# Kernel tuning notes

Measured on AMD Instinct MI355X. Metric: run time of the kernel, lower is better.

Reference implementation:

```python
import jax, jax.numpy as jnp
import numpy as np


def setup_inputs() -> dict:
    key = jax.random.key(0)
    k1, k2, k3 = jax.random.split(key, 3)
    B, C, H, W = 8, 256, 64, 64
    K = jax.random.normal(k1, (B, C, H, W), dtype=jnp.float32)
    Q = jax.random.normal(k2, (B, C, H, W), dtype=jnp.float32)
    V = jax.random.normal(k3, (B, C, H, W), dtype=jnp.float32)
    return {"K": K, "Q": Q, "V": V}


def reference(K, Q, V):
    # K, Q: [b, dim, h, w]; V: [b, v_dim, h, w]
    b, dim, h, w = K.shape
    v_dim = V.shape[1]
    hw = h * w
    Qf = jnp.transpose(K.reshape(b, dim, hw), (0, 2, 1)) * 0  # placeholder removed below
    Qf = jnp.transpose(Q.reshape(b, dim, hw), (0, 2, 1))  # [b, hw, dim]
    Kf = K.reshape(b, dim, hw)                              # [b, dim, hw]
    Vf = jnp.transpose(V.reshape(b, v_dim, hw), (0, 2, 1))  # [b, hw, v_dim]
    scores = jnp.einsum('bqd,bdk->bqk', Qf, Kf)             # [b, hw_q, hw_k]
    # NOTE: softmax over the QUERY axis (dim=1), matching the torch code
    att = jax.nn.softmax(scores, axis=1)
    out = jnp.einsum('bqk,bkv->bqv', att, Vf)               # [b, hw, v_dim]
    out = out.reshape(b, h, w, v_dim)
    return jnp.transpose(out, (0, 3, 1, 2))                 # [b, v_dim, h, w]
```

## Files before the change

### kernel.cpp

```cpp
#include <hip/hip_runtime.h>

#define HW   4096
#define DIM  256
#define NB   8

typedef short bf16x8 __attribute__((ext_vector_type(8)));
typedef short s16x4  __attribute__((ext_vector_type(4)));
typedef float f32x4  __attribute__((ext_vector_type(4)));
typedef float f32x16 __attribute__((ext_vector_type(16)));
typedef unsigned int u32_g __attribute__((address_space(1)));
typedef unsigned int u32_l __attribute__((address_space(3)));

__device__ __forceinline__ void split_bf16(float x, short& hi, short& lo) {
    unsigned u  = __builtin_bit_cast(unsigned, x);
    unsigned rh = (u + 0x7FFFu + ((u >> 16) & 1u)) >> 16;
    hi = (short)rh;
    float hf  = __builtin_bit_cast(float, rh << 16);
    float rem = x - hf;
    unsigned u2 = __builtin_bit_cast(unsigned, rem);
    unsigned rl = (u2 + 0x7FFFu + ((u2 >> 16) & 1u)) >> 16;
    lo = (short)rl;
}

__device__ __forceinline__ f32x4 mfma16(bf16x8 a, bf16x8 b, f32x4 c) {
    return __builtin_amdgcn_mfma_f32_16x16x32_bf16(a, b, c, 0, 0, 0);
}
__device__ __forceinline__ f32x16 mfma32(bf16x8 a, bf16x8 b, f32x16 c) {
    return __builtin_amdgcn_mfma_f32_32x32x16_bf16(a, b, c, 0, 0, 0);
}

__device__ __forceinline__ void gload16(const void* g, void* l) {
    __builtin_amdgcn_global_load_lds((const u32_g*)g, (u32_l*)l, 16, 0, 0);
}
__device__ __forceinline__ void gload4(const void* g, void* l) {
    __builtin_amdgcn_global_load_lds((const u32_g*)g, (u32_l*)l, 4, 0, 0);
}

extern "C" __global__ void __launch_bounds__(256)
pass0_T(const float* __restrict__ src, short* __restrict__ dsth,
        short* __restrict__ dstl)
{
    __shared__ __attribute__((aligned(16))) short TH[16][264];
    __shared__ __attribute__((aligned(16))) short TL[16][264];
    const int b   = blockIdx.y;
    const int hw0 = blockIdx.x * 16;
    const int t   = threadIdx.x;
    const float* sb = src + (size_t)b * DIM * HW;

    {
        const int rl = t & 15;
        const int dl = t >> 4;
        #pragma unroll
        for (int dp = 0; dp < 16; ++dp) {
            int d = dl + dp * 16;
            float x = sb[(size_t)d * HW + hw0 + rl];
            short h, l; split_bf16(x, h, l);
            TH[rl][d] = h; TL[rl][d] = l;
        }
    }
    __syncthreads();

    const int r   = t >> 4;
    const int c0  = (t & 15) * 2;
    const int swz = (r & 7) << 4;
    size_t rowbyte = ((size_t)b * HW + hw0 + r) * (size_t)(DIM * 2);
    char* dh = (char*)dsth + rowbyte;
    char* dl = (char*)dstl + rowbyte;
    #pragma unroll
    for (int j = 0; j < 2; ++j) {
        int cb  = (c0 + j) * 16;
        int cbs = cb ^ swz;
        *(f32x4*)(dh + cbs) = *(const f32x4*)((const char*)&TH[r][0] + cb);
        *(f32x4*)(dl + cbs) = *(const f32x4*)((const char*)&TL[r][0] + cb);
    }
}

extern "C" __global__ void __launch_bounds__(256)
pass0_V(const float* __restrict__ V, short* __restrict__ v2)
{
    const int b = blockIdx.y, v = blockIdx.x, t = threadIdx.x;
    const float* sv = V + ((size_t)b * DIM + v) * HW + t * 16;
    #pragma unroll
    for (int s = 0; s < 2; ++s) {
        f32x4 x0 = *(const f32x4*)(sv + s * 8);
        f32x4 x1 = *(const f32x4*)(sv + s * 8 + 4);
        s16x4 h0, l0, h1, l1;
        #pragma unroll
        for (int j = 0; j < 4; ++j) {
            short h, l;
            split_bf16(x0[j], h, l); h0[j] = h; l0[j] = l;
            split_bf16(x1[j], h, l); h1[j] = h; l1[j] = l;
        }
        short* dp = v2 + (((size_t)b * 512 + (size_t)(t * 2 + s)) * DIM + v) * 16;
        *(s16x4*)(dp + 0)  = h0;
        *(s16x4*)(dp + 4)  = h1;
        *(s16x4*)(dp + 8)  = l0;
        *(s16x4*)(dp + 12) = l1;
    }
}

extern "C" __global__ void __launch_bounds__(512, 2)
k4_stats(const short* __restrict__ KTh, const short* __restrict__ KTl,
         const short* __restrict__ QTh, const short* __restrict__ QTl,
         float* __restrict__ m_out, float* __restrict__ il_out)
{
    __shared__ __attribute__((aligned(16))) short QH[2][64][256];
    __shared__ __attribute__((aligned(16))) short QL[2][64][256];
    __shared__ __attribute__((aligned(16))) float MRG[2][128][2];

    const int id   = blockIdx.x;
    const int b    = id & 7;
    const int k0b  = (id >> 3) * 128;
    const int t    = threadIdx.x;
    const int lane = t & 63;
    const int w    = t >> 6;
    const int l32  = lane & 31;
    const int g2   = lane >> 5;
    const int wk   = w >> 1;
    const int wq   = w & 1;

    bf16x8 kh[16], kl[16];
    {
        const int krow = k0b + wk * 32 + l32;
        const char* rh = (const char*)KTh + ((size_t)b * HW + krow) * 512;
        const char* rl = (const char*)KTl + ((size_t)b * HW + krow) * 512;
        const int swz = (l32 & 7) << 4;
        #pragma unroll
        for (int s = 0; s < 16; ++s) {
            int cb = (s * 32 + g2 * 16) ^ swz;
            kh[s] = *(const bf16x8*)(rh + cb);
            kl[s] = *(const bf16x8*)(rl + cb);
        }
    }

    const char* qhbase = (const char*)QTh + (size_t)b * HW * 512;
    const char* qlbase = (const char*)QTl + (size_t)b * HW * 512;
    auto stage = [&](int bi, int q0) {
        #pragma unroll
        for (int j = 0; j < 4; ++j) {
            int cc = (j << 3) + w;
            int o  = cc * 1024;
            gload16(qhbase + (size_t)q0 * 512 + o + lane * 16,
                    (char*)&QH[bi][0][0] + o);
            gload16(qlbase + (size_t)q0 * 512 + o + lane * 16,
                    (char*)&QL[bi][0][0] + o);
        }
    };

    float mr[16], lr[16];
    #pragma unroll
    for (int r = 0; r < 16; ++r) { mr[r] = -3.0e38f; lr[r] = 0.0f; }

    stage(0, 0);
    __syncthreads();

    const int qrow = wq * 32 + l32;
    const int qswz = (qrow & 7) << 4;

    for (int it = 0; it < 64; ++it) {
        const int cur = it & 1;
        if (it + 1 < 64) stage(cur ^ 1, (it + 1) * 64);

        const char* bhr = (const char*)&QH[cur][qrow][0];
        const char* blr = (const char*)&QL[cur][qrow][0];
        f32x16 c1, c2;
        #pragma unroll
        for (int e = 0; e < 16; ++e) { c1[e] = 0.0f; c2[e] = 0.0f; }

        __builtin_amdgcn_s_setprio(1);
        #pragma unroll
        for (int s = 0; s < 16; ++s) {
            int cb = (s * 32 + g2 * 16) ^ qswz;
            bf16x8 bh = *(const bf16x8*)(bhr + cb);
            bf16x8 bl = *(const bf16x8*)(blr + cb);
            c1 = mfma32(kh[s], bh, c1);
            c1 = mfma32(kh[s], bl, c1);
            c2 = mfma32(kl[s], bh, c2);
        }
        __builtin_amdgcn_s_setprio(0);

        #pragma unroll
        for (int r = 0; r < 16; ++r) {
            float sv = c1[r] + c2[r];
            float nm = fmaxf(mr[r], sv);
            lr[r] = lr[r] * __expf(mr[r] - nm) + __expf(sv - nm);
            mr[r] = nm;
        }
        __syncthreads();
    }

    #pragma unroll
    for (int r = 0; r < 16; ++r) {
        float m = mr[r], l = lr[r];
        #pragma unroll
        for (int off = 1; off < 32; off <<= 1) {
            float m2 = __shfl_xor(m, off);
            float l2 = __shfl_xor(l, off);
            float nm = fmaxf(m, m2);
            l = l * __expf(m - nm) + l2 * __expf(m2 - nm);
            m = nm;
        }
        mr[r] = m; lr[r] = l;
    }
    if (l32 == 0) {
        #pragma unroll
        for (int r = 0; r < 16; ++r) {
            int klo = wk * 32 + 4 * g2 + (r & 3) + 8 * (r >> 2);
            MRG[wq][klo][0] = mr[r];
            MRG[wq][klo][1] = lr[r];
        }
    }
    __syncthreads();
    if (t < 128) {
        float m0 = MRG[0][t][0], l0 = MRG[0][t][1];
        float m1 = MRG[1][t][0], l1 = MRG[1][t][1];
        float nm = fmaxf(m0, m1);
        float l  = l0 * __expf(m0 - nm) + l1 * __expf(m1 - nm);
        m_out[b * HW + k0b + t]  = nm;
        il_out[b * HW + k0b + t] = 1.0f / l;
    }
}

extern "C" __global__ void __launch_bounds__(512, 2)
k4_out(const short* __restrict__ KTh, const short* __restrict__ KTl,
       const short* __restrict__ QTh, const short* __restrict__ QTl,
       const short* __restrict__ V2,
       const float* __restrict__ m_in, const float* __restrict__ il_in,
       float* __restrict__ out)
{
    __shared__ __attribute__((aligned(16))) short KH[64][256];
    __shared__ __attribute__((aligned(16))) short KL[64][256];
    __shared__ __attribute__((aligned(16))) short PH[128][72];
    __shared__ __attribute__((aligned(16))) short PL[128][72];
    __shared__ __attribute__((aligned(16))) float MI[2][128];

    const int id   = blockIdx.x;
    const int b    = id & 7;
    const int q0   = (id >> 3) * 128;
    const int t    = threadIdx.x;
    const int lane = t & 63;
    const int w    = t >> 6;
    const int l32  = lane & 31;
    const int g2   = lane >> 5;
    const int a    = w & 1;
    const int c    = w >> 1;
    const int wv   = w >> 1;
    const int wq2  = w & 1;

    bf16x8 qh[16], ql[16];
    {
        const int qrow = q0 + c * 32 + l32;
        const char* rh = (const char*)QTh + ((size_t)b * HW + qrow) * 512;
        const char* rl = (const char*)QTl + ((size_t)b * HW + qrow) * 512;
        const int swz = (l32 & 7) << 4;
        #pragma unroll
        for (int s = 0; s < 16; ++s) {
            int cb = (s * 32 + g2 * 16) ^ swz;
            qh[s] = *(const bf16x8*)(rh + cb);
            ql[s] = *(const bf16x8*)(rl + cb);
        }
    }

    const char* khbase = (const char*)KTh + (size_t)b * HW * 512;
    const char* klbase = (const char*)KTl + (size_t)b * HW * 512;
    auto stageK = [&](int k0s) {
        #pragma unroll
        for (int j = 0; j < 4; ++j) {
            int cc = (j << 3) + w;
            int o  = cc * 1024;
            gload16(khbase + (size_t)k0s * 512 + o + lane * 16,
                    (char*)&KH[0][0] + o);
            gload16(klbase + (size_t)k0s * 512 + o + lane * 16,
                    (char*)&KL[0][0] + o);
        }
    };
    const float* mB  = m_in  + b * HW;
    const float* ilB = il_in + b * HW;
    auto stageMI = [&](int bi, int k0s) {
        if (w == 0) {
            gload4(mB  + k0s + lane, (char*)&MI[bi][0]);
            gload4(ilB + k0s + lane, (char*)&MI[bi][64]);
        }
    };

    f32x16 acc[2][2];
    #pragma unroll
    for (int i = 0; i < 2; ++i)
        #pragma unroll
        for (int j = 0; j < 2; ++j)
            #pragma unroll
            for (int e = 0; e < 16; ++e) acc[i][j][e] = 0.0f;

    stageK(0);
    stageMI(0, 0);
    __syncthreads();

    const int arow = a * 32 + l32;
    const int aswz = (l32 & 7) << 4;
    const char* ahr = (const char*)&KH[arow][0];
    const char* alr = (const char*)&KL[arow][0];
    const int prow = c * 32 + l32;

    for (int it = 0; it < 64; ++it) {
        const int cur = it & 1;
        const int k0  = it * 64;

        f32x16 c1, c2;
        #pragma unroll
        for (int e = 0; e < 16; ++e) { c1[e] = 0.0f; c2[e] = 0.0f; }

        __builtin_amdgcn_s_setprio(1);
        #pragma unroll
        for (int s = 0; s < 16; ++s) {
            int cb = (s * 32 + g2 * 16) ^ aswz;
            bf16x8 ah = *(const bf16x8*)(ahr + cb);
            bf16x8 al = *(const bf16x8*)(alr + cb);
            c1 = mfma32(ah, qh[s], c1);
            c1 = mfma32(ah, ql[s], c1);
            c2 = mfma32(al, qh[s], c2);
        }
        __builtin_amdgcn_s_setprio(0);

        __syncthreads();

        if (it + 1 < 64) {
            stageK(k0 + 64);
            stageMI(cur ^ 1, k0 + 64);
        }

        #pragma unroll
        for (int run = 0; run < 4; ++run) {
            int idx = a * 32 + 4 * g2 + 8 * run;
            f32x4 m4 = *(const f32x4*)&MI[cur][idx];
            f32x4 i4 = *(const f32x4*)&MI[cur][64 + idx];
            s16x4 ph, pl;
            #pragma unroll
            for (int e = 0; e < 4; ++e) {
                int r = run * 4 + e;
                float sv = c1[r] + c2[r];
                float p  = __expf(sv - m4[e]) * i4[e];
                short h, l; split_bf16(p, h, l);
                ph[e] = h; pl[e] = l;
            }
            *(s16x4*)&PH[prow][idx] = ph;
            *(s16x4*)&PL[prow][idx] = pl;
        }

        __syncthreads();

        __builtin_amdgcn_s_setprio(1);
        #pragma unroll
        for (int kc = 0; kc < 4; ++kc) {
            bf16x8 pbh[2], pbl[2];
            #pragma unroll
            for (int qt = 0; qt < 2; ++qt) {
                int pr = wq2 * 64 + qt * 32 + l32;
                pbh[qt] = *(const bf16x8*)&PH[pr][kc * 16 + g2 * 8];
                pbl[qt] = *(const bf16x8*)&PL[pr][kc * 16 + g2 * 8];
            }
            const int seg = it * 8 + kc * 2 + g2;
            #pragma unroll
            for (int mt = 0; mt < 2; ++mt) {
                int v = wv * 64 + mt * 32 + l32;
                const short* vp = V2 + (((size_t)b * 512 + seg) * DIM + v) * 16;
                bf16x8 vh = *(const bf16x8*)(vp);
                bf16x8 vl = *(const bf16x8*)(vp + 8);
                #pragma unroll
                for (int qt = 0; qt < 2; ++qt) {
                    acc[mt][qt] = mfma32(vh, pbh[qt], acc[mt][qt]);
                    acc[mt][qt] = mfma32(vh, pbl[qt], acc[mt][qt]);
                    acc[mt][qt] = mfma32(vl, pbh[qt], acc[mt][qt]);
                }
            }
        }
        __builtin_amdgcn_s_setprio(0);
    }

    float* __restrict__ ob = out + (size_t)b * DIM * HW;
    #pragma unroll
    for (int mt = 0; mt < 2; ++mt)
        #pragma unroll
        for (int qt = 0; qt < 2; ++qt)
            #pragma unroll
            for (int r = 0; r < 16; ++r) {
                int v = wv * 64 + mt * 32 + (r & 3) + 8 * (r >> 2) + 4 * g2;
                int q = q0 + wq2 * 64 + qt * 32 + l32;
                ob[(size_t)v * HW + q] = acc[mt][qt][r];
            }
}

extern "C" __global__ void __launch_bounds__(256, 1)
k_stats(const float* __restrict__ K, const float* __restrict__ Q,
        float* __restrict__ m_out, float* __restrict__ il_out)
{
    __shared__ __attribute__((aligned(16))) short KtH[64][264];
    __shared__ __attribute__((aligned(16))) short KtL[64][264];
    __shared__ __attribute__((aligned(16))) short QtH[32][264];
    __shared__ __attribute__((aligned(16))) short QtL[32][264];

    const int b = blockIdx.y, k0 = blockIdx.x * 64, t = threadIdx.x;
    const int lane = t & 63, w = t >> 6, g = lane >> 4, lq = lane & 15;
    const float* Kb = K + (size_t)b * DIM * HW;
    const float* Qb = Q + (size_t)b * DIM * HW;

    {
        const int kk = t & 63, d0 = t >> 6;
        #pragma unroll 4
        for (int pass = 0; pass < 64; ++pass) {
            int d = d0 + pass * 4;
            float x = Kb[(size_t)d * HW + k0 + kk];
            short h, l; split_bf16(x, h, l);
            KtH[kk][d] = h; KtL[kk][d] = l;
        }
    }
    float mr[4], lr[4];
    #pragma unroll
    for (int r = 0; r < 4; ++r) { mr[r] = -3.0e38f; lr[r] = 0.0f; }

    for (int q0 = 0; q0 < HW; q0 += 32) {
        __syncthreads();
        {
            const int qq = t & 31, d0 = t >> 5;
            #pragma unroll 4
            for (int pass = 0; pass < 32; ++pass) {
                int d = d0 + pass * 8;
                float x = Qb[(size_t)d * HW + q0 + qq];
                short h, l; split_bf16(x, h, l);
                QtH[qq][d] = h; QtL[qq][d] = l;
            }
        }
        __syncthreads();
        #pragma unroll
        for (int qt = 0; qt < 2; ++qt) {
            f32x4 acc = {0.f, 0.f, 0.f, 0.f};
            #pragma unroll
            for (int ds = 0; ds < 8; ++ds) {
                const int dof = ds * 32 + g * 8;
                bf16x8 ah = *(const bf16x8*)&KtH[w * 16 + lq][dof];
                bf16x8 al = *(const bf16x8*)&KtL[w * 16 + lq][dof];
                bf16x8 bh = *(const bf16x8*)&QtH[qt * 16 + lq][dof];
                bf16x8 bl = *(const bf16x8*)&QtL[qt * 16 + lq][dof];
                acc = mfma16(ah, bh, acc);
                acc = mfma16(ah, bl, acc);
                acc = mfma16(al, bh, acc);
            }
            #pragma unroll
            for (int r = 0; r < 4; ++r) {
                float s = acc[r];
                if (s > mr[r]) { lr[r] = lr[r] * __expf(mr[r] - s) + 1.0f; mr[r] = s; }
                else lr[r] += __expf(s - mr[r]);
            }
        }
    }
    #pragma unroll
    for (int r = 0; r < 4; ++r) {
        float m = mr[r], l = lr[r];
        #pragma unroll
        for (int off = 1; off < 16; off <<= 1) {
            float m2 = __shfl_xor(m, off), l2 = __shfl_xor(l, off);
            float mn = fmaxf(m, m2);
            l = l * __expf(m - mn) + l2 * __expf(m2 - mn);
            m = mn;
        }
        if (lq == 0) {
            int kg = k0 + w * 16 + g * 4 + r;
            m_out[b * HW + kg] = m;
            il_out[b * HW + kg] = 1.0f / l;
        }
    }
}

extern "C" __global__ void __launch_bounds__(256, 1)
k_attn_out(const float* __restrict__ K, const float* __restrict__ Q,
           const float* __restrict__ V,
           const float* __restrict__ m_in, const float* __restrict__ il_in,
           float* __restrict__ out)
{
    __shared__ __attribute__((aligned(16))) short QtH[64][264];
    __shared__ __attribute__((aligned(16))) short QtL[64][264];
    __shared__ __attribute__((aligned(16))) short KtH[32][264];
    __shared__ __attribute__((aligned(16))) short KtL[32][264];
    __shared__ __attribute__((aligned(16))) short PtH[64][40];
    __shared__ __attribute__((aligned(16))) short PtL[64][40];

    const int b = blockIdx.y, q0 = blockIdx.x * 64, t = threadIdx.x;
    const int lane = t & 63, w = t >> 6, g = lane >> 4, lq = lane & 15;
    const int g2 = lane >> 5, l32 = lane & 31;
    const float* Kb = K + (size_t)b * DIM * HW;
    const float* Qb = Q + (size_t)b * DIM * HW;
    const float* Vb = V + (size_t)b * DIM * HW;
    const float* mB = m_in + b * HW;
    const float* ilB = il_in + b * HW;

    {
        const int qq = t & 63, d0 = t >> 6;
        #pragma unroll 4
        for (int pass = 0; pass < 64; ++pass) {
            int d = d0 + pass * 4;
            float x = Qb[(size_t)d * HW + q0 + qq];
            short h, l; split_bf16(x, h, l);
            QtH[qq][d] = h; QtL[qq][d] = l;
        }
    }
    f32x16 acc[2][2];
    #pragma unroll
    for (int i = 0; i < 2; ++i)
        #pragma unroll
        for (int j = 0; j < 2; ++j)
            #pragma unroll
            for (int e = 0; e < 16; ++e) acc[i][j][e] = 0.0f;

    for (int k0 = 0; k0 < HW; k0 += 32) {
        __syncthreads();
        {
            const int kk = t & 31, d0 = t >> 5;
            #pragma unroll 4
            for (int pass = 0; pass < 32; ++pass) {
                int d = d0 + pass * 8;
                float x = Kb[(size_t)d * HW + k0 + kk];
                short h, l; split_bf16(x, h, l);
                KtH[kk][d] = h; KtL[kk][d] = l;
            }
        }
        __syncthreads();
        f32x4 sacc[2];
        #pragma unroll
        for (int kt = 0; kt < 2; ++kt) { f32x4 z = {0.f,0.f,0.f,0.f}; sacc[kt] = z; }
        #pragma unroll
        for (int ds = 0; ds < 8; ++ds) {
            const int dof = ds * 32 + g * 8;
            bf16x8 bh = *(const bf16x8*)&QtH[w * 16 + lq][dof];
            bf16x8 bl = *(const bf16x8*)&QtL[w * 16 + lq][dof];
            #pragma unroll
            for (int kt = 0; kt < 2; ++kt) {
                bf16x8 ah = *(const bf16x8*)&KtH[kt * 16 + lq][dof];
                bf16x8 al = *(const bf16x8*)&KtL[kt * 16 + lq][dof];
                sacc[kt] = mfma16(ah, bh, sacc[kt]);
                sacc[kt] = mfma16(ah, bl, sacc[kt]);
                sacc[kt] = mfma16(al, bh, sacc[kt]);
            }
        }
        {
            const int qc = w * 16 + lq;
            #pragma unroll
            for (int kt = 0; kt < 2; ++kt) {
                s16x4 ph, pl;
                #pragma unroll
                for (int r = 0; r < 4; ++r) {
                    int kg = k0 + kt * 16 + g * 4 + r;
                    float p = __expf(sacc[kt][r] - mB[kg]) * ilB[kg];
                    short h, l; split_bf16(p, h, l);
                    ph[r] = h; pl[r] = l;
                }
                *(s16x4*)&PtH[qc][kt * 16 + g * 4] = ph;
                *(s16x4*)&PtL[qc][kt * 16 + g * 4] = pl;
            }
        }
        __syncthreads();
        #pragma unroll
        for (int kc = 0; kc < 2; ++kc) {
            bf16x8 pbh[2], pbl[2];
            #pragma unroll
            for (int qt = 0; qt < 2; ++qt) {
                pbh[qt] = *(const bf16x8*)&PtH[qt * 32 + l32][kc * 16 + g2 * 8];
                pbl[qt] = *(const bf16x8*)&PtL[qt * 32 + l32][kc * 16 + g2 * 8];
            }
            #pragma unroll
            for (int mt = 0; mt < 2; ++mt) {
                const int v = w * 64 + mt * 32 + l32;
                const float* vp = Vb + (size_t)v * HW + k0 + kc * 16 + g2 * 8;
                f32x4 x0 = *(const f32x4*)vp;
                f32x4 x1 = *(const f32x4*)(vp + 4);
                bf16x8 ah, al;
                #pragma unroll
                for (int j = 0; j < 4; ++j) {
                    short h, l;
                    split_bf16(x0[j], h, l); ah[j] = h;     al[j] = l;
                    split_bf16(x1[j], h, l); ah[4 + j] = h; al[4 + j] = l;
                }
                #pragma unroll
                for (int qt = 0; qt < 2; ++qt) {
                    acc[mt][qt] = mfma32(ah, pbh[qt], acc[mt][qt]);
                    acc[mt][qt] = mfma32(ah, pbl[qt], acc[mt][qt]);
                    acc[mt][qt] = mfma32(al, pbh[qt], acc[mt][qt]);
                }
            }
        }
    }
    float* ob = out + (size_t)b * DIM * HW;
    #pragma unroll
    for (int mt = 0; mt < 2; ++mt)
        #pragma unroll
        for (int qt = 0; qt < 2; ++qt)
            #pragma unroll
            for (int r = 0; r < 16; ++r) {
                int v = w * 64 + mt * 32 + (r & 3) + 8 * (r >> 2) + 4 * g2;
                int q = q0 + qt * 32 + l32;
                ob[(size_t)v * HW + q] = acc[mt][qt][r];
            }
}

extern "C" void kernel_launch(void* const* d_in, const int* in_sizes, int n_in,
                              void* d_out, int out_size, void* d_ws, size_t ws_size,
                              hipStream_t stream)
{
    (void)in_sizes; (void)n_in; (void)out_size;
    const float* K = (const float*)d_in[0];
    const float* Q = (const float*)d_in[1];
    const float* V = (const float*)d_in[2];

    char* wsb = (char*)d_ws;
    float* m_ws  = (float*)wsb;
    float* il_ws = m_ws + (size_t)NB * HW;

    const size_t planeElems = (size_t)NB * HW * DIM;
    const size_t statsBytes = 262144;
    const size_t need = statsBytes + planeElems * 2 * 4
                                   + planeElems * 2 * 2 ;

    dim3 blk(256);
    if (ws_size >= need) {
        short* KTh = (short*)(wsb + statsBytes);
        short* KTl = KTh + planeElems;
        short* QTh = KTl + planeElems;
        short* QTl = QTh + planeElems;
        short* V2  = QTl + planeElems;

        dim3 gT(HW / 16, NB);
        pass0_T<<<gT, blk, 0, stream>>>(K, KTh, KTl);
        pass0_T<<<gT, blk, 0, stream>>>(Q, QTh, QTl);
        dim3 gV(DIM, NB);
        pass0_V<<<gV, blk, 0, stream>>>(V, V2);

        dim3 blk5(512);
        k4_stats<<<dim3(256), blk5, 0, stream>>>(KTh, KTl, QTh, QTl, m_ws, il_ws);
        k4_out<<<dim3(256), blk5, 0, stream>>>(KTh, KTl, QTh, QTl, V2,
                                               m_ws, il_ws, (float*)d_out);
    } else {
        dim3 gM(64, NB);
        k_stats<<<gM, blk, 0, stream>>>(K, Q, m_ws, il_ws);
        k_attn_out<<<gM, blk, 0, stream>>>(K, Q, V, m_ws, il_ws, (float*)d_out);
    }
}
```

Baseline: 710.3 us.

## Stream low-bf16 planes from global in registers, double-buffer K tile in out kernel

The stats and output kernels stop staging the low bf16 half of Q/K in LDS. Instead each wave reads it straight from global memory into registers in groups of four, interleaved with the MFMA chain. This halves LDS traffic and footprint, and the freed space lets the output kernel double-buffer the high K tile so the next tile's prefetch is issued before the current QK compute instead of after a barrier. Other changes: the two score accumulators merge into one, and the P tile row pitch is padded to 68 with split 8-byte LDS reads. The risk is global-load latency stalling the MFMA chain and extra L2 traffic, since each wave re-reads the same low rows.

```diff
diff --git a/kernel.cpp b/kernel.cpp
--- a/kernel.cpp
+++ b/kernel.cpp
@@ -100,12 +100,11 @@
 }
 
 extern "C" __global__ void __launch_bounds__(512, 2)
-k4_stats(const short* __restrict__ KTh, const short* __restrict__ KTl,
+k6_stats(const short* __restrict__ KTh, const short* __restrict__ KTl,
          const short* __restrict__ QTh, const short* __restrict__ QTl,
          float* __restrict__ m_out, float* __restrict__ il_out)
 {
     __shared__ __attribute__((aligned(16))) short QH[2][64][256];
-    __shared__ __attribute__((aligned(16))) short QL[2][64][256];
     __shared__ __attribute__((aligned(16))) float MRG[2][128][2];
 
     const int id   = blockIdx.x;
@@ -135,15 +134,25 @@
 
     const char* qhbase = (const char*)QTh + (size_t)b * HW * 512;
     const char* qlbase = (const char*)QTl + (size_t)b * HW * 512;
-    auto stage = [&](int bi, int q0) {
+    auto stage = [&](int bi, int q0s) {
         #pragma unroll
         for (int j = 0; j < 4; ++j) {
             int cc = (j << 3) + w;
             int o  = cc * 1024;
-            gload16(qhbase + (size_t)q0 * 512 + o + lane * 16,
+            gload16(qhbase + (size_t)q0s * 512 + o + lane * 16,
                     (char*)&QH[bi][0][0] + o);
-            gload16(qlbase + (size_t)q0 * 512 + o + lane * 16,
-                    (char*)&QL[bi][0][0] + o);
+        }
+    };
+
+    const int qrow = wq * 32 + l32;
+    const int qswz = (qrow & 7) << 4;
+
+    auto LOADB = [&](bf16x8* buf, int sg, const char* rowp) {
+        #pragma unroll
+        for (int e = 0; e < 4; ++e) {
+            const int s = sg * 4 + e;
+            int cb = (s * 32 + g2 * 16) ^ qswz;
+            buf[e] = *(const bf16x8*)(rowp + cb);
         }
     };
 
@@ -153,35 +162,44 @@
 
     stage(0, 0);
     __syncthreads();
-
-    const int qrow = wq * 32 + l32;
-    const int qswz = (qrow & 7) << 4;
 
     for (int it = 0; it < 64; ++it) {
         const int cur = it & 1;
         if (it + 1 < 64) stage(cur ^ 1, (it + 1) * 64);
 
-        const char* bhr = (const char*)&QH[cur][qrow][0];
-        const char* blr = (const char*)&QL[cur][qrow][0];
-        f32x16 c1, c2;
-        #pragma unroll
-        for (int e = 0; e < 16; ++e) { c1[e] = 0.0f; c2[e] = 0.0f; }
+        const char* blrow = qlbase + (size_t)(it * 64 + qrow) * 512;
+        const char* bhr   = (const char*)&QH[cur][qrow][0];
+
+        bf16x8 blA[4], blB[4];
+        LOADB(blA, 0, blrow);
+        LOADB(blB, 1, blrow);
+
+        f32x16 cS;
+        #pragma unroll
+        for (int e = 0; e < 16; ++e) cS[e] = 0.0f;
+
+        auto SGRP = [&](const bf16x8* blbuf, int sg) {
+            #pragma unroll
+            for (int e = 0; e < 4; ++e) {
+                const int s = sg * 4 + e;
+                int cb = (s * 32 + g2 * 16) ^ qswz;
+                bf16x8 bh = *(const bf16x8*)(bhr + cb);
+                cS = mfma32(kh[s], bh, cS);
+                cS = mfma32(kh[s], blbuf[e], cS);
+                cS = mfma32(kl[s], bh, cS);
+            }
+        };
 
         __builtin_amdgcn_s_setprio(1);
-        #pragma unroll
-        for (int s = 0; s < 16; ++s) {
-            int cb = (s * 32 + g2 * 16) ^ qswz;
-            bf16x8 bh = *(const bf16x8*)(bhr + cb);
-            bf16x8 bl = *(const bf16x8*)(blr + cb);
-            c1 = mfma32(kh[s], bh, c1);
-            c1 = mfma32(kh[s], bl, c1);
-            c2 = mfma32(kl[s], bh, c2);
-        }
+        SGRP(blA, 0); LOADB(blA, 2, blrow);
+        SGRP(blB, 1); LOADB(blB, 3, blrow);
+        SGRP(blA, 2);
+        SGRP(blB, 3);
         __builtin_amdgcn_s_setprio(0);
 
         #pragma unroll
         for (int r = 0; r < 16; ++r) {
-            float sv = c1[r] + c2[r];
+            float sv = cS[r];
             float nm = fmaxf(mr[r], sv);
             lr[r] = lr[r] * __expf(mr[r] - nm) + __expf(sv - nm);
             mr[r] = nm;
@@ -222,16 +240,15 @@
 }
 
 extern "C" __global__ void __launch_bounds__(512, 2)
-k4_out(const short* __restrict__ KTh, const short* __restrict__ KTl,
+k6_out(const short* __restrict__ KTh, const short* __restrict__ KTl,
        const short* __restrict__ QTh, const short* __restrict__ QTl,
        const short* __restrict__ V2,
        const float* __restrict__ m_in, const float* __restrict__ il_in,
        float* __restrict__ out)
 {
-    __shared__ __attribute__((aligned(16))) short KH[64][256];
-    __shared__ __attribute__((aligned(16))) short KL[64][256];
-    __shared__ __attribute__((aligned(16))) short PH[128][72];
-    __shared__ __attribute__((aligned(16))) short PL[128][72];
+    __shared__ __attribute__((aligned(16))) short KH[2][64][256];
+    __shared__ __attribute__((aligned(16))) short PH[128][68];
+    __shared__ __attribute__((aligned(16))) short PL[128][68];
     __shared__ __attribute__((aligned(16))) float MI[2][128];
 
     const int id   = blockIdx.x;
@@ -263,15 +280,13 @@
 
     const char* khbase = (const char*)KTh + (size_t)b * HW * 512;
     const char* klbase = (const char*)KTl + (size_t)b * HW * 512;
-    auto stageK = [&](int k0s) {
+    auto stageK = [&](int bi, int k0s) {
         #pragma unroll
         for (int j = 0; j < 4; ++j) {
             int cc = (j << 3) + w;
             int o  = cc * 1024;
             gload16(khbase + (size_t)k0s * 512 + o + lane * 16,
-                    (char*)&KH[0][0] + o);
-            gload16(klbase + (size_t)k0s * 512 + o + lane * 16,
-                    (char*)&KL[0][0] + o);
+                    (char*)&KH[bi][0][0] + o);
         }
     };
     const float* mB  = m_in  + b * HW;
@@ -291,42 +306,62 @@
             #pragma unroll
             for (int e = 0; e < 16; ++e) acc[i][j][e] = 0.0f;
 
-    stageK(0);
+    stageK(0, 0);
     stageMI(0, 0);
     __syncthreads();
 
     const int arow = a * 32 + l32;
     const int aswz = (l32 & 7) << 4;
-    const char* ahr = (const char*)&KH[arow][0];
-    const char* alr = (const char*)&KL[arow][0];
     const int prow = c * 32 + l32;
+
+    auto LOADA = [&](bf16x8* buf, int sg, const char* rowp) {
+        #pragma unroll
+        for (int e = 0; e < 4; ++e) {
+            const int s = sg * 4 + e;
+            int cb = (s * 32 + g2 * 16) ^ aswz;
+            buf[e] = *(const bf16x8*)(rowp + cb);
+        }
+    };
 
     for (int it = 0; it < 64; ++it) {
         const int cur = it & 1;
         const int k0  = it * 64;
 
-        f32x16 c1, c2;
-        #pragma unroll
-        for (int e = 0; e < 16; ++e) { c1[e] = 0.0f; c2[e] = 0.0f; }
+        if (it + 1 < 64) {
+            stageK(cur ^ 1, k0 + 64);
+            stageMI(cur ^ 1, k0 + 64);
+        }
+
+        const char* alrow = klbase + (size_t)(k0 + arow) * 512;
+        bf16x8 alA[4], alB[4];
+        LOADA(alA, 0, alrow);
+        LOADA(alB, 1, alrow);
+
+        const char* ahr = (const char*)&KH[cur][arow][0];
+        f32x16 cS;
+        #pragma unroll
+        for (int e = 0; e < 16; ++e) cS[e] = 0.0f;
+
+        auto SGRP = [&](const bf16x8* albuf, int sg) {
+            #pragma unroll
+            for (int e = 0; e < 4; ++e) {
+                const int s = sg * 4 + e;
+                int cb = (s * 32 + g2 * 16) ^ aswz;
+                bf16x8 ah = *(const bf16x8*)(ahr + cb);
+                cS = mfma32(ah, qh[s], cS);
+                cS = mfma32(ah, ql[s], cS);
+                cS = mfma32(albuf[e], qh[s], cS);
+            }
+        };
 
         __builtin_amdgcn_s_setprio(1);
-        #pragma unroll
-        for (int s = 0; s < 16; ++s) {
-            int cb = (s * 32 + g2 * 16) ^ aswz;
-            bf16x8 ah = *(const bf16x8*)(ahr + cb);
-            bf16x8 al = *(const bf16x8*)(alr + cb);
-            c1 = mfma32(ah, qh[s], c1);
-            c1 = mfma32(ah, ql[s], c1);
-            c2 = mfma32(al, qh[s], c2);
-        }
+        SGRP(alA, 0); LOADA(alA, 2, alrow);
+        SGRP(alB, 1); LOADA(alB, 3, alrow);
+        SGRP(alA, 2);
+        SGRP(alB, 3);
         __builtin_amdgcn_s_setprio(0);
 
         __syncthreads();
-
-        if (it + 1 < 64) {
-            stageK(k0 + 64);
-            stageMI(cur ^ 1, k0 + 64);
-        }
 
         #pragma unroll
         for (int run = 0; run < 4; ++run) {
@@ -337,8 +372,7 @@
             #pragma unroll
             for (int e = 0; e < 4; ++e) {
                 int r = run * 4 + e;
-                float sv = c1[r] + c2[r];
-                float p  = __expf(sv - m4[e]) * i4[e];
+                float p = __expf(cS[r] - m4[e]) * i4[e];
                 short h, l; split_bf16(p, h, l);
                 ph[e] = h; pl[e] = l;
             }
@@ -355,8 +389,14 @@
             #pragma unroll
             for (int qt = 0; qt < 2; ++qt) {
                 int pr = wq2 * 64 + qt * 32 + l32;
-                pbh[qt] = *(const bf16x8*)&PH[pr][kc * 16 + g2 * 8];
-                pbl[qt] = *(const bf16x8*)&PL[pr][kc * 16 + g2 * 8];
+                const short* p0 = &PH[pr][kc * 16 + g2 * 8];
+                const short* p1 = &PL[pr][kc * 16 + g2 * 8];
+                s16x4 a0 = *(const s16x4*)(p0);
+                s16x4 a1 = *(const s16x4*)(p0 + 4);
+                s16x4 b0 = *(const s16x4*)(p1);
+                s16x4 b1 = *(const s16x4*)(p1 + 4);
+                pbh[qt] = __builtin_shufflevector(a0, a1, 0, 1, 2, 3, 4, 5, 6, 7);
+                pbl[qt] = __builtin_shufflevector(b0, b1, 0, 1, 2, 3, 4, 5, 6, 7);
             }
             const int seg = it * 8 + kc * 2 + g2;
             #pragma unroll
@@ -633,8 +673,8 @@
         pass0_V<<<gV, blk, 0, stream>>>(V, V2);
 
         dim3 blk5(512);
-        k4_stats<<<dim3(256), blk5, 0, stream>>>(KTh, KTl, QTh, QTl, m_ws, il_ws);
-        k4_out<<<dim3(256), blk5, 0, stream>>>(KTh, KTl, QTh, QTl, V2,
+        k6_stats<<<dim3(256), blk5, 0, stream>>>(KTh, KTl, QTh, QTl, m_ws, il_ws);
+        k6_out<<<dim3(256), blk5, 0, stream>>>(KTh, KTl, QTh, QTl, V2,
                                                m_ws, il_ws, (float*)d_out);
     } else {
         dim3 gM(64, NB);
```

After: 1.181 ms. 66.2% more time.
